# Kernel tuning notes

Hardware: AMD Instinct MI355X
Metric: run time of the kernel (lower is better)

The kernel has to match this reference:

```python
import jax, jax.numpy as jnp
import numpy as np


def setup_inputs() -> dict:
    key = jax.random.key(0)
    k1, k2 = jax.random.split(key)
    B, Tq, Tk, D = 8, 2048, 2048, 1024
    query = jax.random.normal(k1, (B, Tq, D), dtype=jnp.float32)
    key_t = jax.random.normal(k2, (B, Tk, D), dtype=jnp.float32)
    return {"query": query, "key": key_t}


def reference(query, key):
    # Unscaled cross attention: key acts as both K and V.
    # energy: [B, Tq, Tk]
    energy = jnp.einsum("bqd,bkd->bqk", query, key)
    attention = jax.nn.softmax(energy, axis=-1)
    # output: [B, Tq, D]
    return jnp.einsum("bqk,bkd->bqd", attention, key)
```

## Files before the change

### kernel.cpp

```cpp
#include <hip/hip_runtime.h>
#include <stdint.h>

typedef int i32x4 __attribute__((ext_vector_type(4)));
typedef int8_t s8;

__device__ __forceinline__ void gload_lds16(const void* g, uint32_t lds_addr) {
  __builtin_amdgcn_global_load_lds(
      (const __attribute__((address_space(1))) void*)(uintptr_t)g,
      (__attribute__((address_space(3))) void*)(uintptr_t)lds_addr,
      16, 0, 0);
}

__device__ __forceinline__ void qsplit(float x, float s, float sinv, float s2inv,
                                       int& q1, int& q2) {
  float a = rintf(x * sinv);
  a = fminf(fmaxf(a, -127.f), 127.f);
  float r = fmaf(a, -s, x);
  float b = fminf(fmaxf(rintf(r * s2inv), -127.f), 127.f);
  q1 = (int)a; q2 = (int)b;
}
__device__ __forceinline__ uint32_t pack4(int b0, int b1, int b2, int b3) {
  return ((uint32_t)(uint8_t)b0) | ((uint32_t)(uint8_t)b1 << 8) |
         ((uint32_t)(uint8_t)b2 << 16) | ((uint32_t)(uint8_t)b3 << 24);
}

#define SQ (8.0f / 127.0f)
#define SQ_INV 15.875f
#define SQ2_INV 2032.0f

__global__ __launch_bounds__(256) void cvt_q_i8(const float* __restrict__ x,
                                                s8* __restrict__ a, s8* __restrict__ b) {
  size_t i = ((size_t)blockIdx.x * 256 + threadIdx.x) * 8;
  float4 v0 = ((const float4*)(x + i))[0];
  float4 v1 = ((const float4*)(x + i))[1];
  float f[8] = {v0.x, v0.y, v0.z, v0.w, v1.x, v1.y, v1.z, v1.w};
  int q1[8], q2[8];
#pragma unroll
  for (int j = 0; j < 8; j++) qsplit(f[j], SQ, SQ_INV, SQ2_INV, q1[j], q2[j]);
  uint2 ua, ub;
  ua.x = pack4(q1[0], q1[1], q1[2], q1[3]); ua.y = pack4(q1[4], q1[5], q1[6], q1[7]);
  ub.x = pack4(q2[0], q2[1], q2[2], q2[3]); ub.y = pack4(q2[4], q2[5], q2[6], q2[7]);
  *(uint2*)(a + i) = ua;
  *(uint2*)(b + i) = ub;
}

__global__ __launch_bounds__(256) void cvt_k_i8(const float* __restrict__ K,
                                                s8* __restrict__ k1, s8* __restrict__ k2,
                                                s8* __restrict__ t1, s8* __restrict__ t2) {
  __shared__ uint32_t tile[64][33];
  const int b = blockIdx.z;
  const int d0 = blockIdx.x * 32, t0 = blockIdx.y * 64;
  const int tid = threadIdx.x;
  const float* Kb = K + (size_t)b * 2048 * 1024;
  {
    const int t = tid >> 2, d8 = (tid & 3) * 8;
    const float* src = Kb + (size_t)(t0 + t) * 1024 + d0 + d8;
    float4 v0 = ((const float4*)src)[0];
    float4 v1 = ((const float4*)src)[1];
    float f[8] = {v0.x, v0.y, v0.z, v0.w, v1.x, v1.y, v1.z, v1.w};
    int q1[8], q2[8];
#pragma unroll
    for (int j = 0; j < 8; j++) {
      qsplit(f[j], SQ, SQ_INV, SQ2_INV, q1[j], q2[j]);
      tile[t][d8 + j] = ((uint32_t)(uint8_t)q1[j]) | ((uint32_t)(uint8_t)q2[j] << 8);
    }
    uint2 ua, ub;
    ua.x = pack4(q1[0], q1[1], q1[2], q1[3]); ua.y = pack4(q1[4], q1[5], q1[6], q1[7]);
    ub.x = pack4(q2[0], q2[1], q2[2], q2[3]); ub.y = pack4(q2[4], q2[5], q2[6], q2[7]);
    size_t off = (size_t)b * 2048 * 1024 + (size_t)(t0 + t) * 1024 + d0 + d8;
    *(uint2*)(k1 + off) = ua;
    *(uint2*)(k2 + off) = ub;
  }
  __syncthreads();
  {
    const int d = tid >> 3, tg = tid & 7;
    uint32_t v[8];
#pragma unroll
    for (int i = 0; i < 8; i++) v[i] = tile[tg * 8 + i][d];
    uint2 ua, ub;
    ua.x = pack4(v[0], v[1], v[2], v[3]); ua.y = pack4(v[4], v[5], v[6], v[7]);
    ub.x = pack4(v[0] >> 8, v[1] >> 8, v[2] >> 8, v[3] >> 8);
    ub.y = pack4(v[4] >> 8, v[5] >> 8, v[6] >> 8, v[7] >> 8);
    size_t off = (size_t)b * 1024 * 2048 + (size_t)(d0 + d) * 2048 + t0 + tg * 8;
    *(uint2*)(t1 + off) = ua;
    *(uint2*)(t2 + off) = ub;
  }
}

__global__ __launch_bounds__(256) void softmax_i8(const float* __restrict__ E,
                                                  s8* __restrict__ P1, s8* __restrict__ P2) {
  const size_t row = blockIdx.x;
  const float* e = E + row * 2048;
  const int t = threadIdx.x;
  float4 a = ((const float4*)e)[t * 2];
  float4 b = ((const float4*)e)[t * 2 + 1];
  float f[8] = {a.x, a.y, a.z, a.w, b.x, b.y, b.z, b.w};
  float m = f[0];
#pragma unroll
  for (int j = 1; j < 8; j++) m = fmaxf(m, f[j]);
#pragma unroll
  for (int off = 32; off > 0; off >>= 1) m = fmaxf(m, __shfl_down(m, off));
  __shared__ float redm[4], reds[4];
  if ((t & 63) == 0) redm[t >> 6] = m;
  __syncthreads();
  m = fmaxf(fmaxf(redm[0], redm[1]), fmaxf(redm[2], redm[3]));
  float ex[8];
  float s = 0.f;
#pragma unroll
  for (int j = 0; j < 8; j++) { ex[j] = __expf(f[j] - m); s += ex[j]; }
#pragma unroll
  for (int off = 32; off > 0; off >>= 1) s += __shfl_down(s, off);
  if ((t & 63) == 0) reds[t >> 6] = s;
  __syncthreads();
  s = reds[0] + reds[1] + reds[2] + reds[3];
  float inv = 1.0f / s;
  int q1[8], q2[8];
#pragma unroll
  for (int j = 0; j < 8; j++)
    qsplit(ex[j] * inv, 1.0f / 127.0f, 127.0f, 16256.0f, q1[j], q2[j]);
  uint2 ua, ub;
  ua.x = pack4(q1[0], q1[1], q1[2], q1[3]); ua.y = pack4(q1[4], q1[5], q1[6], q1[7]);
  ub.x = pack4(q2[0], q2[1], q2[2], q2[3]); ub.y = pack4(q2[4], q2[5], q2[6], q2[7]);
  *(uint2*)(P1 + row * 2048 + t * 8) = ua;
  *(uint2*)(P2 + row * 2048 + t * 8) = ub;
}

__global__ __launch_bounds__(256, 2) void gemm_i8(
    const s8* __restrict__ A0, const s8* __restrict__ A1,
    const s8* __restrict__ B0, const s8* __restrict__ B1,
    float* __restrict__ C, int Kdim, int ldc, long sA, long sB, long sC,
    float c1, float c2) {
  __shared__ char lds[2][32768];
  const int tid = threadIdx.x;
  const int w = tid >> 6, l = tid & 63;

  const int gx = gridDim.x, gy = gridDim.y;
  const int nwg = gx * gy * gridDim.z;
  const int f = (blockIdx.z * gy + blockIdx.y) * gx + blockIdx.x;
  const int cpx = nwg >> 3;
  const int swz = (f & 7) * cpx + (f >> 3);
  const int bandsz = 8 * gy;
  const int band = swz / bandsz, r = swz % bandsz;
  const int nbx = gx >> 3;
  const int bx = (band % nbx) * 8 + (r & 7);
  const int by = r >> 3;
  const int bz = band / nbx;

  const int rowA = by * 128, rowB = bx * 128;
  const s8* bases[4] = {A0 + bz * sA, A1 + bz * sA, B0 + bz * sB, B1 + bz * sB};
  const int rbase[4] = {rowA, rowA, rowB, rowB};
  const s8* gp[8];
  uint32_t lpo[8];
#pragma unroll
  for (int i = 0; i < 8; i++) {
    int gc = w * 8 + i;
    int buf = gc >> 3, c = gc & 7;
    int row = c * 16 + (l >> 2);
    int q = (l & 3) ^ ((row >> 1) & 3);
    gp[i] = bases[buf] + (size_t)(rbase[buf] + row) * Kdim + q * 16;
    lpo[i] = (uint32_t)(uintptr_t)(&lds[0][0] + buf * 8192 + c * 1024 + l * 16);
  }
  i32x4 acc1[4][4], acc2[4][4];
  const i32x4 zero = {0, 0, 0, 0};
#pragma unroll
  for (int mt = 0; mt < 4; mt++)
#pragma unroll
    for (int nt = 0; nt < 4; nt++) { acc1[mt][nt] = zero; acc2[mt][nt] = zero; }

  const int wm = w & 1, wn = w >> 1, q4 = l >> 4, rl = l & 15;

#pragma unroll
  for (int i = 0; i < 8; i++) { gload_lds16(gp[i], lpo[i]); gp[i] += 64; }

  int cur = 0;
  for (int k0 = 0; k0 < Kdim; k0 += 64) {
    __builtin_amdgcn_s_barrier();
    if (k0 + 64 < Kdim) {
      const uint32_t nb = (uint32_t)(cur ^ 1) * 32768u;
#pragma unroll
      for (int i = 0; i < 8; i++) { gload_lds16(gp[i], lpo[i] + nb); gp[i] += 64; }
      asm volatile("s_waitcnt vmcnt(8)" ::: "memory");
    } else {
      asm volatile("s_waitcnt vmcnt(0)" ::: "memory");
    }
    __builtin_amdgcn_sched_barrier(0);
    __builtin_amdgcn_s_barrier();
    const char* L = &lds[cur][0];
    i32x4 af0[4], af1[4];
#pragma unroll
    for (int mt = 0; mt < 4; mt++) {
      int row = wm * 64 + mt * 16 + rl;
      int off = row * 64 + ((q4 ^ ((row >> 1) & 3)) << 4);
      af0[mt] = *(const i32x4*)(L + off);
      af1[mt] = *(const i32x4*)(L + 8192 + off);
    }
    __builtin_amdgcn_s_setprio(1);
#pragma unroll
    for (int nt = 0; nt < 4; nt++) {
      int row = wn * 64 + nt * 16 + rl;
      int off = row * 64 + ((q4 ^ ((row >> 1) & 3)) << 4);
      i32x4 bf0 = *(const i32x4*)(L + 16384 + off);
      i32x4 bf1 = *(const i32x4*)(L + 24576 + off);
#pragma unroll
      for (int mt = 0; mt < 4; mt++) {
        acc1[mt][nt] = __builtin_amdgcn_mfma_i32_16x16x64_i8(af0[mt], bf0, acc1[mt][nt], 0, 0, 0);
        acc2[mt][nt] = __builtin_amdgcn_mfma_i32_16x16x64_i8(af0[mt], bf1, acc2[mt][nt], 0, 0, 0);
        acc2[mt][nt] = __builtin_amdgcn_mfma_i32_16x16x64_i8(af1[mt], bf0, acc2[mt][nt], 0, 0, 0);
      }
    }
    __builtin_amdgcn_s_setprio(0);
    cur ^= 1;
  }
  float* Cb = C + (size_t)bz * sC + (size_t)rowA * ldc + rowB;
#pragma unroll
  for (int mt = 0; mt < 4; mt++)
#pragma unroll
    for (int nt = 0; nt < 4; nt++)
#pragma unroll
      for (int r2 = 0; r2 < 4; r2++)
        Cb[(size_t)(wm * 64 + mt * 16 + q4 * 4 + r2) * ldc + (wn * 64 + nt * 16 + rl)] =
            c1 * (float)acc1[mt][nt][r2] + c2 * (float)acc2[mt][nt][r2];
}

extern "C" void kernel_launch(void* const* d_in, const int* in_sizes, int n_in,
                              void* d_out, int out_size, void* d_ws, size_t ws_size,
                              hipStream_t stream) {
  (void)in_sizes; (void)n_in; (void)out_size;
  const float* Q = (const float*)d_in[0];
  const float* K = (const float*)d_in[1];
  float* O = (float*)d_out;
  const int Btot = 8, Tq = 2048, Tk = 2048, D = 1024;
  const size_t perb = 36ull << 20;
  int NB = 8;
  while (NB > 1 && (size_t)NB * perb > ws_size) NB >>= 1;

  char* p = (char*)d_ws;
  const size_t qd = (size_t)NB * Tq * D;
  const size_t kd = (size_t)NB * Tk * D;
  const size_t ee = (size_t)NB * Tq * Tk;
  s8* Q1 = (s8*)p; p += qd;
  s8* Q2 = (s8*)p; p += qd;
  s8* K1 = (s8*)p; p += kd;
  s8* K2 = (s8*)p; p += kd;
  s8* KT1 = (s8*)p; p += kd;
  s8* KT2 = (s8*)p; p += kd;
  float* E = (float*)p; p += ee * 4;
  s8* P1 = (s8*)p; p += ee;
  s8* P2 = (s8*)p; p += ee;

  const float g1c1 = 64.0f / 16129.0f, g1c2 = g1c1 * (1.0f / 128.0f);
  const float g2c1 = 8.0f / 16129.0f, g2c2 = g2c1 * (1.0f / 128.0f);

  for (int c = 0; c < Btot / NB; c++) {
    const float* Qc = Q + (size_t)c * qd;
    const float* Kc = K + (size_t)c * kd;
    float* Oc = O + (size_t)c * qd;
    cvt_q_i8<<<dim3(NB * 1024), 256, 0, stream>>>(Qc, Q1, Q2);
    cvt_k_i8<<<dim3(32, 32, NB), 256, 0, stream>>>(Kc, K1, K2, KT1, KT2);
    gemm_i8<<<dim3(16, 16, NB), 256, 0, stream>>>(
        Q1, Q2, K1, K2, E, 1024, 2048, (long)Tq * D, (long)Tk * D, (long)Tq * Tk,
        g1c1, g1c2);
    softmax_i8<<<dim3(NB * Tq), 256, 0, stream>>>(E, P1, P2);
    gemm_i8<<<dim3(8, 16, NB), 256, 0, stream>>>(
        P1, P2, KT1, KT2, Oc, 2048, 1024, (long)Tq * Tk, (long)D * Tk, (long)Tq * D,
        g2c1, g2c2);
  }
}
```

Measured before the change: 404.3 us.

## Interleave global-to-LDS prefetch issues across MFMA phases in int8 GEMM loop

Splits the eight per-iteration global_load_lds prefetches into four pairs, issuing them between the four MFMA N-tile phases instead of all at once at the top of the loop. The point is to spread VMEM issue across compute and so reduce issue burstiness and contention. It adds extra workgroup barriers between phases and an explicit lgkmcnt wait per phase, which may add synchronisation stalls. The vmcnt wait is adjusted to account for only the first pair being in flight.

```diff
diff --git a/kernel.cpp b/kernel.cpp
--- a/kernel.cpp
+++ b/kernel.cpp
@@ -172,19 +172,45 @@
 #pragma unroll
   for (int i = 0; i < 8; i++) { gload_lds16(gp[i], lpo[i]); gp[i] += 64; }
 
+#define STAGE2(i0, i1)                                         \
+  do {                                                         \
+    gload_lds16(gp[i0], lpo[i0] + nb); gp[i0] += 64;           \
+    gload_lds16(gp[i1], lpo[i1] + nb); gp[i1] += 64;           \
+  } while (0)
+
+#define GPHASE(p, STAGE_STMT)                                                  \
+  {                                                                            \
+    int row_ = wn * 64 + (p) * 16 + rl;                                        \
+    int off_ = row_ * 64 + ((q4 ^ ((row_ >> 1) & 3)) << 4);                    \
+    i32x4 bf0 = *(const i32x4*)(L + 16384 + off_);                             \
+    i32x4 bf1 = *(const i32x4*)(L + 24576 + off_);                             \
+    if (pf) { STAGE_STMT; }                                                    \
+    asm volatile("s_waitcnt lgkmcnt(0)" ::: "memory");                         \
+    __builtin_amdgcn_sched_barrier(0);                                         \
+    __builtin_amdgcn_s_setprio(1);                                             \
+    _Pragma("unroll")                                                          \
+    for (int mt = 0; mt < 4; mt++) {                                           \
+      acc1[mt][p] = __builtin_amdgcn_mfma_i32_16x16x64_i8(af0[mt], bf0, acc1[mt][p], 0, 0, 0); \
+      acc2[mt][p] = __builtin_amdgcn_mfma_i32_16x16x64_i8(af0[mt], bf1, acc2[mt][p], 0, 0, 0); \
+      acc2[mt][p] = __builtin_amdgcn_mfma_i32_16x16x64_i8(af1[mt], bf0, acc2[mt][p], 0, 0, 0); \
+    }                                                                          \
+    __builtin_amdgcn_s_setprio(0);                                             \
+  }
+
   int cur = 0;
   for (int k0 = 0; k0 < Kdim; k0 += 64) {
-    __builtin_amdgcn_s_barrier();
-    if (k0 + 64 < Kdim) {
-      const uint32_t nb = (uint32_t)(cur ^ 1) * 32768u;
-#pragma unroll
-      for (int i = 0; i < 8; i++) { gload_lds16(gp[i], lpo[i] + nb); gp[i] += 64; }
-      asm volatile("s_waitcnt vmcnt(8)" ::: "memory");
+    const bool pf = (k0 + 64 < Kdim);
+    const uint32_t nb = (uint32_t)(cur ^ 1) * 32768u;
+    __builtin_amdgcn_s_barrier();
+    if (pf) {
+      STAGE2(0, 1);
+      asm volatile("s_waitcnt vmcnt(2)" ::: "memory");
     } else {
       asm volatile("s_waitcnt vmcnt(0)" ::: "memory");
     }
     __builtin_amdgcn_sched_barrier(0);
     __builtin_amdgcn_s_barrier();
+    __builtin_amdgcn_sched_barrier(0);
     const char* L = &lds[cur][0];
     i32x4 af0[4], af1[4];
 #pragma unroll
@@ -194,23 +220,17 @@
       af0[mt] = *(const i32x4*)(L + off);
       af1[mt] = *(const i32x4*)(L + 8192 + off);
     }
-    __builtin_amdgcn_s_setprio(1);
-#pragma unroll
-    for (int nt = 0; nt < 4; nt++) {
-      int row = wn * 64 + nt * 16 + rl;
-      int off = row * 64 + ((q4 ^ ((row >> 1) & 3)) << 4);
-      i32x4 bf0 = *(const i32x4*)(L + 16384 + off);
-      i32x4 bf1 = *(const i32x4*)(L + 24576 + off);
-#pragma unroll
-      for (int mt = 0; mt < 4; mt++) {
-        acc1[mt][nt] = __builtin_amdgcn_mfma_i32_16x16x64_i8(af0[mt], bf0, acc1[mt][nt], 0, 0, 0);
-        acc2[mt][nt] = __builtin_amdgcn_mfma_i32_16x16x64_i8(af0[mt], bf1, acc2[mt][nt], 0, 0, 0);
-        acc2[mt][nt] = __builtin_amdgcn_mfma_i32_16x16x64_i8(af1[mt], bf0, acc2[mt][nt], 0, 0, 0);
-      }
-    }
-    __builtin_amdgcn_s_setprio(0);
+    GPHASE(0, STAGE2(2, 3));
+    __builtin_amdgcn_s_barrier();
+    GPHASE(1, STAGE2(4, 5));
+    __builtin_amdgcn_s_barrier();
+    GPHASE(2, STAGE2(6, 7));
+    __builtin_amdgcn_s_barrier();
+    GPHASE(3, ((void)0));
     cur ^= 1;
   }
+#undef GPHASE
+#undef STAGE2
   float* Cb = C + (size_t)bz * sC + (size_t)rowA * ldc + rowB;
 #pragma unroll
   for (int mt = 0; mt < 4; mt++)
```

Result: faster. 386.1 us (-4.5%).
